# Kernel optimization log

Hardware: AMD Instinct MI355X
Metric: run time of the kernel (lower is better)

The kernel has to match this reference:

```python
import jax, jax.numpy as jnp
import numpy as np

B, S, D, E2 = 64, 512, 1024, 1024  # batch, enc seq len, dec hidden, 2*enc hidden


def setup_inputs() -> dict:
    key = jax.random.key(0)
    ks = jax.random.split(key, 5)
    scale = 1.0 / np.sqrt(D + E2)
    return {
        "dec_state": jax.random.normal(ks[0], (B, D), jnp.float32),
        "enc_states": jax.random.normal(ks[1], (B, S, E2), jnp.float32),
        "att_mask": jnp.ones((B, S), jnp.int32),
        "w_weight": jax.random.normal(ks[2], (D, D + E2), jnp.float32) * scale,
        "w_bias": jax.random.normal(ks[3], (D,), jnp.float32) * scale,
        "v_weight": jax.random.normal(ks[4], (D,), jnp.float32) * (1.0 / np.sqrt(D)),
    }


def reference(dec_state, enc_states, att_mask, w_weight, w_bias, v_weight):
    # Additive (Bahdanau) attention. Split the concat-linear into two GEMMs:
    # tanh(W [dec; enc] + b) == tanh(dec @ Wd^T + enc @ We^T + b) -- same math,
    # avoids materializing the repeated/concatenated [B,S,D+2E] tensor.
    Wd = w_weight[:, :dec_state.shape[-1]]          # [D, D]
    We = w_weight[:, dec_state.shape[-1]:]          # [D, 2E]
    dec_proj = jnp.einsum('bd,kd->bk', dec_state, Wd)        # [B, D]
    enc_proj = jnp.einsum('bse,ke->bsk', enc_states, We)     # [B, S, D]
    energy = jnp.tanh(enc_proj + dec_proj[:, None, :] + w_bias)  # [B, S, D]
    attention = jnp.einsum('bsk,k->bs', energy, v_weight)    # [B, S]
    attention = jnp.where(att_mask == 0, -jnp.inf, attention)
    att_weights = jax.nn.softmax(attention, axis=1)          # [B, S]
    att_out = jnp.einsum('bs,bse->be', att_weights, enc_states)[:, None, :]  # [B,1,2E]
    return att_out
```

## Files before the change

### kernel.cpp

```cpp
#include <hip/hip_runtime.h>
#include <hip/hip_bf16.h>
#include <math.h>

#define B_  64
#define S_  512
#define D_  1024
#define E2_ 1024
#define WROW (D_ + E2_)
#define NTILES 4

typedef __attribute__((ext_vector_type(8))) short bf16x8;
typedef __attribute__((ext_vector_type(4))) float f32x4;
typedef __attribute__((ext_vector_type(8))) unsigned short u16x8;

__device__ __forceinline__ unsigned short f2bf(float f) {
    unsigned u = __float_as_uint(f);
    u = (u + 0x7FFFu + ((u >> 16) & 1u)) >> 16;
    return (unsigned short)u;
}

__device__ __forceinline__ void load_lds16(const void* g, void* l) {
    __builtin_amdgcn_global_load_lds(
        (__attribute__((address_space(1))) void*)(void*)g,
        (__attribute__((address_space(3))) void*)l,
        16, 0, 0);
}

__device__ __forceinline__ float fast_tanh(float x) {
    float ax = fminf(fabsf(x), 16.0f);
    float t  = __builtin_amdgcn_exp2f(ax * 2.8853900817779268f);
    float r  = (t - 1.0f) * __builtin_amdgcn_rcpf(t + 1.0f);
    return copysignf(r, x);
}

__global__ __launch_bounds__(256) void conv_we_kernel(
        const float* __restrict__ w, unsigned short* __restrict__ web)
{
    const int k = blockIdx.x;
    const int j = threadIdx.x * 4;
    float4 a = *reinterpret_cast<const float4*>(w + (size_t)k * WROW + D_ + j);
    ushort4 o;
    o.x = f2bf(a.x); o.y = f2bf(a.y); o.z = f2bf(a.z); o.w = f2bf(a.w);
    *reinterpret_cast<ushort4*>(web + (size_t)k * E2_ + j) = o;
}

__global__ __launch_bounds__(256) void dec_proj_kernel(
        const float* __restrict__ dec,
        const float* __restrict__ w,
        const float* __restrict__ bias,
        float* __restrict__ t)
{
    __shared__ float wrow[D_];
    __shared__ float red[256];
    const int k = blockIdx.x;
    const int tid = threadIdx.x;

    const float* wr = w + (size_t)k * WROW;
    for (int i = tid; i < D_; i += 256) wrow[i] = wr[i];
    __syncthreads();

    const int b = tid >> 2;
    const int q = tid & 3;
    const float* dp = dec + b * D_ + q * 256;
    const float* wp = wrow + q * 256;
    float acc = 0.f;
    #pragma unroll 8
    for (int i = 0; i < 256; ++i) acc = fmaf(dp[i], wp[i], acc);
    red[tid] = acc;
    __syncthreads();
    if (q == 0) {
        float s = red[tid] + red[tid + 1] + red[tid + 2] + red[tid + 3];
        t[b * D_ + k] = s + bias[k];
    }
}

#define BME 256
#define BNE 256
#define BKE 64
#define KT_ (E2_ / BKE)

__global__ __launch_bounds__(512, 2) void energy_mfma_kernel(
        const float* __restrict__ encf,
        const unsigned short* __restrict__ web,
        const float* __restrict__ t,
        const float* __restrict__ v,
        float* __restrict__ att_part)
{
    __shared__ __align__(16) unsigned short As[2][BME * BKE];
    __shared__ __align__(16) unsigned short Bs[2][BNE * BKE];
    __shared__ float tv_s[BNE];
    __shared__ float vv_s[BNE];
    __shared__ float red[4][BME];

    const int g     = blockIdx.x;
    const int mblk  = (g & 7) + 8 * (g >> 5);
    const int ntile = (g >> 3) & 3;

    const int m0 = mblk * BME;
    const int n0 = ntile * BNE;
    const int b  = m0 >> 9;
    const int tid = threadIdx.x;
    const int w   = tid >> 6;
    const int l   = tid & 63;
    const int wm  = w >> 2;
    const int wn  = w & 3;

    if (tid < BNE) {
        tv_s[tid] = t[b * D_ + n0 + tid];
        vv_s[tid] = v[n0 + tid];
    }

    const int arow0 = tid >> 4;
    const int acolb = (tid & 15) * 8;
    const int aswz  = (arow0 & 7) << 4;
    const float* gAf = encf + (size_t)m0 * E2_;

    const int lr8 = l >> 3;
    const int lk  = 8 * ((l & 7) ^ lr8);
    const unsigned short* gB = web + (size_t)n0 * E2_;

    const int rA = wm * 128 + (l & 15);
    const int rB = wn * 64 + (l & 15);
    const int kswz = (l & 7) << 4;
    const int khi  = (l >> 4) << 4;

    f32x4 acc[8][4] = {};
    float4 av[8];

    auto issueA = [&](int kt) {
        const int k0 = kt * BKE;
        #pragma unroll
        for (int i = 0; i < 8; ++i) {
            const int row = i * 32 + arow0;
            av[i] = *reinterpret_cast<const float4*>(
                gAf + (size_t)row * E2_ + k0 + (tid & 15) * 4);
        }
    };
    auto writeA = [&](int bf) {
        #pragma unroll
        for (int i = 0; i < 8; ++i) {
            const int row = i * 32 + arow0;
            unsigned p0, p1;
            asm("v_cvt_pk_bf16_f32 %0, %1, %2"
                : "=v"(p0) : "v"(av[i].x), "v"(av[i].y));
            asm("v_cvt_pk_bf16_f32 %0, %1, %2"
                : "=v"(p1) : "v"(av[i].z), "v"(av[i].w));
            uint2 o; o.x = p0; o.y = p1;
            *reinterpret_cast<uint2*>(
                (char*)As[bf] + row * 128 + (acolb ^ aswz)) = o;
        }
    };
    auto issueB = [&](int bf, int kt) {
        const int k0 = kt * BKE;
        #pragma unroll
        for (int r = 0; r < 4; ++r) {
            const int c = r * 8 + w;
            const int row = c * 8 + lr8;
            load_lds16(gB + (size_t)row * E2_ + k0 + lk,
                       (char*)Bs[bf] + c * 1024);
        }
    };

    issueA(0);
    issueB(0, 0);
    writeA(0);
    issueA(1);
    asm volatile("s_waitcnt vmcnt(8) lgkmcnt(0)" ::: "memory");
    __builtin_amdgcn_s_barrier();
    __builtin_amdgcn_sched_barrier(0);

    for (int kt = 0; kt < KT_; ++kt) {
        const int cur = kt & 1;
        const int nxt = cur ^ 1;

        if (kt + 1 < KT_) issueB(nxt, kt + 1);
        __builtin_amdgcn_sched_barrier(0);

        {
            const int kb = khi ^ kswz;
            bf16x8 a[8], bb[4];
            #pragma unroll
            for (int mi = 0; mi < 8; ++mi)
                a[mi] = *reinterpret_cast<const bf16x8*>(
                    (const char*)As[cur] + (rA + mi * 16) * 128 + kb);
            #pragma unroll
            for (int ni = 0; ni < 4; ++ni)
                bb[ni] = *reinterpret_cast<const bf16x8*>(
                    (const char*)Bs[cur] + (rB + ni * 16) * 128 + kb);
            __builtin_amdgcn_s_setprio(1);
            #pragma unroll
            for (int mi = 0; mi < 8; ++mi)
                #pragma unroll
                for (int ni = 0; ni < 4; ++ni)
                    acc[mi][ni] = __builtin_amdgcn_mfma_f32_16x16x32_bf16(
                        a[mi], bb[ni], acc[mi][ni], 0, 0, 0);
            __builtin_amdgcn_s_setprio(0);
        }
        __builtin_amdgcn_sched_barrier(0);

        if (kt + 1 < KT_) writeA(nxt);
        if (kt + 2 < KT_) issueA(kt + 2);
        __builtin_amdgcn_sched_barrier(0);

        {
            const int kb = (64 + khi) ^ kswz;
            bf16x8 a[8], bb[4];
            #pragma unroll
            for (int mi = 0; mi < 8; ++mi)
                a[mi] = *reinterpret_cast<const bf16x8*>(
                    (const char*)As[cur] + (rA + mi * 16) * 128 + kb);
            #pragma unroll
            for (int ni = 0; ni < 4; ++ni)
                bb[ni] = *reinterpret_cast<const bf16x8*>(
                    (const char*)Bs[cur] + (rB + ni * 16) * 128 + kb);
            __builtin_amdgcn_s_setprio(1);
            #pragma unroll
            for (int mi = 0; mi < 8; ++mi)
                #pragma unroll
                for (int ni = 0; ni < 4; ++ni)
                    acc[mi][ni] = __builtin_amdgcn_mfma_f32_16x16x32_bf16(
                        a[mi], bb[ni], acc[mi][ni], 0, 0, 0);
            __builtin_amdgcn_s_setprio(0);
        }
        __builtin_amdgcn_sched_barrier(0);

        if (kt + 2 < KT_) {
            asm volatile("s_waitcnt vmcnt(8) lgkmcnt(0)" ::: "memory");
        } else if (kt + 1 < KT_) {
            asm volatile("s_waitcnt vmcnt(0) lgkmcnt(0)" ::: "memory");
        }
        __builtin_amdgcn_s_barrier();
        __builtin_amdgcn_sched_barrier(0);
    }

    #pragma unroll
    for (int mi = 0; mi < 8; ++mi) {
        float P[4] = {0.f, 0.f, 0.f, 0.f};
        #pragma unroll
        for (int ni = 0; ni < 4; ++ni) {
            const int nl = wn * 64 + ni * 16 + (l & 15);
            const float tvv = tv_s[nl];
            const float vvv = vv_s[nl];
            #pragma unroll
            for (int j = 0; j < 4; ++j) {
                float e = fast_tanh(acc[mi][ni][j] + tvv);
                P[j] = fmaf(e, vvv, P[j]);
            }
        }
        #pragma unroll
        for (int j = 0; j < 4; ++j) {
            float p = P[j];
            p += __shfl_xor(p, 1);
            p += __shfl_xor(p, 2);
            p += __shfl_xor(p, 4);
            p += __shfl_xor(p, 8);
            if ((l & 15) == 0)
                red[wn][wm * 128 + mi * 16 + (l >> 4) * 4 + j] = p;
        }
    }
    __syncthreads();
    if (tid < BME)
        att_part[(size_t)(m0 + tid) * NTILES + ntile] =
            (red[0][tid] + red[1][tid]) + (red[2][tid] + red[3][tid]);
}

__global__ __launch_bounds__(256) void softmax_kernel(
        const float* __restrict__ att_part,
        const int* __restrict__ mask,
        float* __restrict__ wout)
{
    __shared__ float red[256];
    const int b = blockIdx.x;
    const int tid = threadIdx.x;

    float x0 = 0.f, x1 = 0.f;
    #pragma unroll
    for (int p = 0; p < NTILES; ++p) {
        x0 += att_part[(size_t)(b * S_ + tid) * NTILES + p];
        x1 += att_part[(size_t)(b * S_ + 256 + tid) * NTILES + p];
    }
    bool m0v = (mask[b * S_ + tid] != 0);
    bool m1v = (mask[b * S_ + 256 + tid] != 0);
    if (!m0v) x0 = -INFINITY;
    if (!m1v) x1 = -INFINITY;

    float m = fmaxf(x0, x1);
    red[tid] = m;
    __syncthreads();
    for (int o = 128; o > 0; o >>= 1) {
        if (tid < o) red[tid] = fmaxf(red[tid], red[tid + o]);
        __syncthreads();
    }
    m = red[0];
    __syncthreads();

    float e0 = m0v ? expf(x0 - m) : 0.f;
    float e1 = m1v ? expf(x1 - m) : 0.f;
    red[tid] = e0 + e1;
    __syncthreads();
    for (int o = 128; o > 0; o >>= 1) {
        if (tid < o) red[tid] += red[tid + o];
        __syncthreads();
    }
    const float inv = 1.f / red[0];
    wout[b * S_ + tid] = e0 * inv;
    wout[b * S_ + 256 + tid] = e1 * inv;
}

__global__ __launch_bounds__(256) void attout_part_kernel(
        const float* __restrict__ wgt,
        const float* __restrict__ enc,
        float* __restrict__ out_part)
{
    __shared__ float wsm[64];
    const int b  = blockIdx.y;
    const int sc = blockIdx.x;
    const int tid = threadIdx.x;
    if (tid < 64) wsm[tid] = wgt[b * S_ + sc * 64 + tid];
    __syncthreads();

    const float4* ep = reinterpret_cast<const float4*>(
        enc + ((size_t)b * S_ + sc * 64) * E2_) + tid;
    float4 acc = {0.f, 0.f, 0.f, 0.f};
    #pragma unroll 8
    for (int s = 0; s < 64; ++s) {
        float4 e4 = ep[(size_t)s * (E2_ / 4)];
        const float ws = wsm[s];
        acc.x = fmaf(ws, e4.x, acc.x);
        acc.y = fmaf(ws, e4.y, acc.y);
        acc.z = fmaf(ws, e4.z, acc.z);
        acc.w = fmaf(ws, e4.w, acc.w);
    }
    reinterpret_cast<float4*>(out_part + ((size_t)sc * B_ + b) * E2_)[tid] = acc;
}

__global__ __launch_bounds__(256) void attout_reduce_kernel(
        const float* __restrict__ out_part,
        float* __restrict__ out)
{
    const int idx = blockIdx.x * 256 + threadIdx.x;
    const int n4 = (B_ * E2_) / 4;
    const float4* p = reinterpret_cast<const float4*>(out_part);
    float4 r = p[idx];
    #pragma unroll
    for (int c = 1; c < 8; ++c) {
        float4 q = p[idx + c * n4];
        r.x += q.x; r.y += q.y; r.z += q.z; r.w += q.w;
    }
    reinterpret_cast<float4*>(out)[idx] = r;
}

extern "C" void kernel_launch(void* const* d_in, const int* in_sizes, int n_in,
                              void* d_out, int out_size, void* d_ws, size_t ws_size,
                              hipStream_t stream) {
    const float* dec  = (const float*)d_in[0];
    const float* enc  = (const float*)d_in[1];
    const int*   mask = (const int*)d_in[2];
    const float* w    = (const float*)d_in[3];
    const float* bias = (const float*)d_in[4];
    const float* v    = (const float*)d_in[5];
    float* out = (float*)d_out;

    float* t_buf    = (float*)d_ws;
    float* att_part = t_buf + B_ * D_;
    float* wgt_buf  = att_part + B_ * S_ * NTILES;
    float* out_part = wgt_buf + B_ * S_;
    unsigned short* web = (unsigned short*)(out_part + 8 * B_ * E2_);

    conv_we_kernel<<<D_, 256, 0, stream>>>(w, web);
    dec_proj_kernel<<<D_, 256, 0, stream>>>(dec, w, bias, t_buf);
    energy_mfma_kernel<<<512, 512, 0, stream>>>(enc, web, t_buf, v, att_part);
    softmax_kernel<<<B_, 256, 0, stream>>>(att_part, mask, wgt_buf);
    attout_part_kernel<<<dim3(8, B_), 256, 0, stream>>>(wgt_buf, enc, out_part);
    attout_reduce_kernel<<<(B_ * E2_ / 4) / 256, 256, 0, stream>>>(out_part, out);
}
```

Before: 143.1 us.

## Fuse prep kernels, write bf16 enc copy in energy GEMM, fuse softmax into attout

Merges the weight conversion and dec projection into one launch and folds the softmax into the attention-output kernel, which recomputes it per block. The energy GEMM now writes a bf16 copy of enc_states from its ntile==0 blocks, so the weighted sum reads half the bytes. It also drops the min-blocks hint from the GEMM launch bounds. This removes two launches and cuts the second full read of enc, at the cost of extra global stores inside the GEMM, a possible register or occupancy change, and bf16 rounding in the output sum.

```diff
diff --git a/kernel.cpp b/kernel.cpp
--- a/kernel.cpp
+++ b/kernel.cpp
@@ -19,6 +19,10 @@
     return (unsigned short)u;
 }
 
+__device__ __forceinline__ float bf2f(unsigned short u) {
+    return __uint_as_float((unsigned)u << 16);
+}
+
 __device__ __forceinline__ void load_lds16(const void* g, void* l) {
     __builtin_amdgcn_global_load_lds(
         (__attribute__((address_space(1))) void*)(void*)g,
@@ -33,44 +37,44 @@
     return copysignf(r, x);
 }
 
-__global__ __launch_bounds__(256) void conv_we_kernel(
-        const float* __restrict__ w, unsigned short* __restrict__ web)
-{
-    const int k = blockIdx.x;
-    const int j = threadIdx.x * 4;
-    float4 a = *reinterpret_cast<const float4*>(w + (size_t)k * WROW + D_ + j);
-    ushort4 o;
-    o.x = f2bf(a.x); o.y = f2bf(a.y); o.z = f2bf(a.z); o.w = f2bf(a.w);
-    *reinterpret_cast<ushort4*>(web + (size_t)k * E2_ + j) = o;
-}
-
-__global__ __launch_bounds__(256) void dec_proj_kernel(
+__global__ __launch_bounds__(256) void prep_kernel(
+        const float* __restrict__ w,
         const float* __restrict__ dec,
-        const float* __restrict__ w,
         const float* __restrict__ bias,
+        unsigned short* __restrict__ web,
         float* __restrict__ t)
 {
-    __shared__ float wrow[D_];
-    __shared__ float red[256];
-    const int k = blockIdx.x;
+    const int blk = blockIdx.x;
     const int tid = threadIdx.x;
 
-    const float* wr = w + (size_t)k * WROW;
-    for (int i = tid; i < D_; i += 256) wrow[i] = wr[i];
-    __syncthreads();
-
-    const int b = tid >> 2;
-    const int q = tid & 3;
-    const float* dp = dec + b * D_ + q * 256;
-    const float* wp = wrow + q * 256;
-    float acc = 0.f;
-    #pragma unroll 8
-    for (int i = 0; i < 256; ++i) acc = fmaf(dp[i], wp[i], acc);
-    red[tid] = acc;
-    __syncthreads();
-    if (q == 0) {
-        float s = red[tid] + red[tid + 1] + red[tid + 2] + red[tid + 3];
-        t[b * D_ + k] = s + bias[k];
+    if (blk < D_) {
+        const int k = blk;
+        const int j = tid * 4;
+        float4 a = *reinterpret_cast<const float4*>(w + (size_t)k * WROW + D_ + j);
+        ushort4 o;
+        o.x = f2bf(a.x); o.y = f2bf(a.y); o.z = f2bf(a.z); o.w = f2bf(a.w);
+        *reinterpret_cast<ushort4*>(web + (size_t)k * E2_ + j) = o;
+    } else {
+        __shared__ float wrow[D_];
+        __shared__ float red[256];
+        const int k = blk - D_;
+        const float* wr = w + (size_t)k * WROW;
+        for (int i = tid; i < D_; i += 256) wrow[i] = wr[i];
+        __syncthreads();
+
+        const int b = tid >> 2;
+        const int q = tid & 3;
+        const float* dp = dec + b * D_ + q * 256;
+        const float* wp = wrow + q * 256;
+        float acc = 0.f;
+        #pragma unroll 8
+        for (int i = 0; i < 256; ++i) acc = fmaf(dp[i], wp[i], acc);
+        red[tid] = acc;
+        __syncthreads();
+        if (q == 0) {
+            float s = red[tid] + red[tid + 1] + red[tid + 2] + red[tid + 3];
+            t[b * D_ + k] = s + bias[k];
+        }
     }
 }
 
@@ -79,12 +83,13 @@
 #define BKE 64
 #define KT_ (E2_ / BKE)
 
-__global__ __launch_bounds__(512, 2) void energy_mfma_kernel(
+__global__ __launch_bounds__(512) void energy_mfma_kernel(
         const float* __restrict__ encf,
         const unsigned short* __restrict__ web,
         const float* __restrict__ t,
         const float* __restrict__ v,
-        float* __restrict__ att_part)
+        float* __restrict__ att_part,
+        unsigned short* __restrict__ encb)
 {
     __shared__ __align__(16) unsigned short As[2][BME * BKE];
     __shared__ __align__(16) unsigned short Bs[2][BNE * BKE];
@@ -104,6 +109,7 @@
     const int l   = tid & 63;
     const int wm  = w >> 2;
     const int wn  = w & 3;
+    const bool do_store = (ntile == 0);
 
     if (tid < BNE) {
         tv_s[tid] = t[b * D_ + n0 + tid];
@@ -114,6 +120,7 @@
     const int acolb = (tid & 15) * 8;
     const int aswz  = (arow0 & 7) << 4;
     const float* gAf = encf + (size_t)m0 * E2_;
+    unsigned short* gOut = encb + (size_t)m0 * E2_;
 
     const int lr8 = l >> 3;
     const int lk  = 8 * ((l & 7) ^ lr8);
@@ -136,7 +143,8 @@
                 gAf + (size_t)row * E2_ + k0 + (tid & 15) * 4);
         }
     };
-    auto writeA = [&](int bf) {
+    auto writeA = [&](int bf, int kt) {
+        const int k0 = kt * BKE;
         #pragma unroll
         for (int i = 0; i < 8; ++i) {
             const int row = i * 32 + arow0;
@@ -148,6 +156,9 @@
             uint2 o; o.x = p0; o.y = p1;
             *reinterpret_cast<uint2*>(
                 (char*)As[bf] + row * 128 + (acolb ^ aswz)) = o;
+            if (do_store)
+                *reinterpret_cast<uint2*>(
+                    gOut + (size_t)row * E2_ + k0 + (tid & 15) * 4) = o;
         }
     };
     auto issueB = [&](int bf, int kt) {
@@ -163,7 +174,7 @@
 
     issueA(0);
     issueB(0, 0);
-    writeA(0);
+    writeA(0, 0);
     issueA(1);
     asm volatile("s_waitcnt vmcnt(8) lgkmcnt(0)" ::: "memory");
     __builtin_amdgcn_s_barrier();
@@ -198,7 +209,7 @@
         }
         __builtin_amdgcn_sched_barrier(0);
 
-        if (kt + 1 < KT_) writeA(nxt);
+        if (kt + 1 < KT_) writeA(nxt, kt + 1);
         if (kt + 2 < KT_) issueA(kt + 2);
         __builtin_amdgcn_sched_barrier(0);
 
@@ -264,74 +275,70 @@
             (red[0][tid] + red[1][tid]) + (red[2][tid] + red[3][tid]);
 }
 
-__global__ __launch_bounds__(256) void softmax_kernel(
+__global__ __launch_bounds__(128) void attout_sm_kernel(
         const float* __restrict__ att_part,
         const int* __restrict__ mask,
-        float* __restrict__ wout)
-{
-    __shared__ float red[256];
-    const int b = blockIdx.x;
-    const int tid = threadIdx.x;
-
-    float x0 = 0.f, x1 = 0.f;
-    #pragma unroll
-    for (int p = 0; p < NTILES; ++p) {
-        x0 += att_part[(size_t)(b * S_ + tid) * NTILES + p];
-        x1 += att_part[(size_t)(b * S_ + 256 + tid) * NTILES + p];
-    }
-    bool m0v = (mask[b * S_ + tid] != 0);
-    bool m1v = (mask[b * S_ + 256 + tid] != 0);
-    if (!m0v) x0 = -INFINITY;
-    if (!m1v) x1 = -INFINITY;
-
-    float m = fmaxf(x0, x1);
-    red[tid] = m;
-    __syncthreads();
-    for (int o = 128; o > 0; o >>= 1) {
-        if (tid < o) red[tid] = fmaxf(red[tid], red[tid + o]);
-        __syncthreads();
-    }
-    m = red[0];
-    __syncthreads();
-
-    float e0 = m0v ? expf(x0 - m) : 0.f;
-    float e1 = m1v ? expf(x1 - m) : 0.f;
-    red[tid] = e0 + e1;
-    __syncthreads();
-    for (int o = 128; o > 0; o >>= 1) {
-        if (tid < o) red[tid] += red[tid + o];
-        __syncthreads();
-    }
-    const float inv = 1.f / red[0];
-    wout[b * S_ + tid] = e0 * inv;
-    wout[b * S_ + 256 + tid] = e1 * inv;
-}
-
-__global__ __launch_bounds__(256) void attout_part_kernel(
-        const float* __restrict__ wgt,
-        const float* __restrict__ enc,
+        const unsigned short* __restrict__ encb,
         float* __restrict__ out_part)
 {
-    __shared__ float wsm[64];
+    __shared__ float wall[S_];
+    __shared__ float red[128];
     const int b  = blockIdx.y;
     const int sc = blockIdx.x;
     const int tid = threadIdx.x;
-    if (tid < 64) wsm[tid] = wgt[b * S_ + sc * 64 + tid];
-    __syncthreads();
-
-    const float4* ep = reinterpret_cast<const float4*>(
-        enc + ((size_t)b * S_ + sc * 64) * E2_) + tid;
-    float4 acc = {0.f, 0.f, 0.f, 0.f};
-    #pragma unroll 8
+
+    float x[4];
+    bool mv[4];
+    #pragma unroll
+    for (int j = 0; j < 4; ++j) {
+        const int s = tid + j * 128;
+        float4 p = *reinterpret_cast<const float4*>(
+            att_part + (size_t)(b * S_ + s) * NTILES);
+        x[j] = (p.x + p.y) + (p.z + p.w);
+        mv[j] = (mask[b * S_ + s] != 0);
+        if (!mv[j]) x[j] = -INFINITY;
+    }
+    float m = fmaxf(fmaxf(x[0], x[1]), fmaxf(x[2], x[3]));
+    red[tid] = m;
+    __syncthreads();
+    for (int o = 64; o > 0; o >>= 1) {
+        if (tid < o) red[tid] = fmaxf(red[tid], red[tid + o]);
+        __syncthreads();
+    }
+    m = red[0];
+    __syncthreads();
+    float e[4], esum = 0.f;
+    #pragma unroll
+    for (int j = 0; j < 4; ++j) {
+        e[j] = mv[j] ? expf(x[j] - m) : 0.f;
+        esum += e[j];
+    }
+    red[tid] = esum;
+    __syncthreads();
+    for (int o = 64; o > 0; o >>= 1) {
+        if (tid < o) red[tid] += red[tid + o];
+        __syncthreads();
+    }
+    const float inv = 1.f / red[0];
+    #pragma unroll
+    for (int j = 0; j < 4; ++j) wall[tid + j * 128] = e[j] * inv;
+    __syncthreads();
+
+    const float* wsm = wall + sc * 64;
+    const unsigned short* ep =
+        encb + ((size_t)b * S_ + sc * 64) * E2_ + tid * 8;
+    float acc[8] = {};
+    #pragma unroll 4
     for (int s = 0; s < 64; ++s) {
-        float4 e4 = ep[(size_t)s * (E2_ / 4)];
+        u16x8 e8 = *reinterpret_cast<const u16x8*>(ep + (size_t)s * E2_);
         const float ws = wsm[s];
-        acc.x = fmaf(ws, e4.x, acc.x);
-        acc.y = fmaf(ws, e4.y, acc.y);
-        acc.z = fmaf(ws, e4.z, acc.z);
-        acc.w = fmaf(ws, e4.w, acc.w);
-    }
-    reinterpret_cast<float4*>(out_part + ((size_t)sc * B_ + b) * E2_)[tid] = acc;
+        #pragma unroll
+        for (int j = 0; j < 8; ++j)
+            acc[j] = fmaf(ws, bf2f((unsigned short)e8[j]), acc[j]);
+    }
+    float* op = out_part + ((size_t)sc * B_ + b) * E2_ + tid * 8;
+    #pragma unroll
+    for (int j = 0; j < 8; ++j) op[j] = acc[j];
 }
 
 __global__ __launch_bounds__(256) void attout_reduce_kernel(
@@ -363,14 +370,14 @@
 
     float* t_buf    = (float*)d_ws;
     float* att_part = t_buf + B_ * D_;
-    float* wgt_buf  = att_part + B_ * S_ * NTILES;
-    float* out_part = wgt_buf + B_ * S_;
-    unsigned short* web = (unsigned short*)(out_part + 8 * B_ * E2_);
-
-    conv_we_kernel<<<D_, 256, 0, stream>>>(w, web);
-    dec_proj_kernel<<<D_, 256, 0, stream>>>(dec, w, bias, t_buf);
-    energy_mfma_kernel<<<512, 512, 0, stream>>>(enc, web, t_buf, v, att_part);
-    softmax_kernel<<<B_, 256, 0, stream>>>(att_part, mask, wgt_buf);
-    attout_part_kernel<<<dim3(8, B_), 256, 0, stream>>>(wgt_buf, enc, out_part);
+    float* out_part = att_part + B_ * S_ * NTILES;
+    unsigned short* web  = (unsigned short*)(out_part + 8 * B_ * E2_);
+    unsigned short* encb = web + (size_t)D_ * E2_;
+
+    prep_kernel<<<2 * D_, 256, 0, stream>>>(w, dec, bias, web, t_buf);
+    energy_mfma_kernel<<<512, 512, 0, stream>>>(enc, web, t_buf, v,
+                                                att_part, encb);
+    attout_sm_kernel<<<dim3(8, B_), 128, 0, stream>>>(att_part, mask,
+                                                      encb, out_part);
     attout_reduce_kernel<<<(B_ * E2_ / 4) / 256, 256, 0, stream>>>(out_part, out);
 }
```

Result: no change. 141.5 us (-1.1%).

## Merge prep kernels and fuse softmax into attention-output partial kernel

Applied to the files above, without the earlier changes.

Combines the weight bf16 conversion and the decoder projection into one launch, with each block choosing its role from its index. Folds the softmax into the attention-output partial kernel: every (chunk, batch) block recomputes the full-row softmax in shared memory, which removes the separate softmax launch and the weight buffer round trip. It also vectorises the partial-score loads and drops the min-blocks-per-CU hint on the energy GEMM. The cost is that the softmax is computed redundantly eight times per batch row, and the GEMM may end up with different register allocation and occupancy.

```diff
diff --git a/kernel.cpp b/kernel.cpp
--- a/kernel.cpp
+++ b/kernel.cpp
@@ -33,44 +33,44 @@
     return copysignf(r, x);
 }
 
-__global__ __launch_bounds__(256) void conv_we_kernel(
-        const float* __restrict__ w, unsigned short* __restrict__ web)
-{
-    const int k = blockIdx.x;
-    const int j = threadIdx.x * 4;
-    float4 a = *reinterpret_cast<const float4*>(w + (size_t)k * WROW + D_ + j);
-    ushort4 o;
-    o.x = f2bf(a.x); o.y = f2bf(a.y); o.z = f2bf(a.z); o.w = f2bf(a.w);
-    *reinterpret_cast<ushort4*>(web + (size_t)k * E2_ + j) = o;
-}
-
-__global__ __launch_bounds__(256) void dec_proj_kernel(
+__global__ __launch_bounds__(256) void prep_kernel(
+        const float* __restrict__ w,
         const float* __restrict__ dec,
-        const float* __restrict__ w,
         const float* __restrict__ bias,
+        unsigned short* __restrict__ web,
         float* __restrict__ t)
 {
-    __shared__ float wrow[D_];
-    __shared__ float red[256];
-    const int k = blockIdx.x;
+    const int blk = blockIdx.x;
     const int tid = threadIdx.x;
 
-    const float* wr = w + (size_t)k * WROW;
-    for (int i = tid; i < D_; i += 256) wrow[i] = wr[i];
-    __syncthreads();
-
-    const int b = tid >> 2;
-    const int q = tid & 3;
-    const float* dp = dec + b * D_ + q * 256;
-    const float* wp = wrow + q * 256;
-    float acc = 0.f;
-    #pragma unroll 8
-    for (int i = 0; i < 256; ++i) acc = fmaf(dp[i], wp[i], acc);
-    red[tid] = acc;
-    __syncthreads();
-    if (q == 0) {
-        float s = red[tid] + red[tid + 1] + red[tid + 2] + red[tid + 3];
-        t[b * D_ + k] = s + bias[k];
+    if (blk < D_) {
+        const int k = blk;
+        const int j = tid * 4;
+        float4 a = *reinterpret_cast<const float4*>(w + (size_t)k * WROW + D_ + j);
+        ushort4 o;
+        o.x = f2bf(a.x); o.y = f2bf(a.y); o.z = f2bf(a.z); o.w = f2bf(a.w);
+        *reinterpret_cast<ushort4*>(web + (size_t)k * E2_ + j) = o;
+    } else {
+        __shared__ float wrow[D_];
+        __shared__ float red[256];
+        const int k = blk - D_;
+        const float* wr = w + (size_t)k * WROW;
+        for (int i = tid; i < D_; i += 256) wrow[i] = wr[i];
+        __syncthreads();
+
+        const int b = tid >> 2;
+        const int q = tid & 3;
+        const float* dp = dec + b * D_ + q * 256;
+        const float* wp = wrow + q * 256;
+        float acc = 0.f;
+        #pragma unroll 8
+        for (int i = 0; i < 256; ++i) acc = fmaf(dp[i], wp[i], acc);
+        red[tid] = acc;
+        __syncthreads();
+        if (q == 0) {
+            float s = red[tid] + red[tid + 1] + red[tid + 2] + red[tid + 3];
+            t[b * D_ + k] = s + bias[k];
+        }
     }
 }
 
@@ -79,7 +79,7 @@
 #define BKE 64
 #define KT_ (E2_ / BKE)
 
-__global__ __launch_bounds__(512, 2) void energy_mfma_kernel(
+__global__ __launch_bounds__(512) void energy_mfma_kernel(
         const float* __restrict__ encf,
         const unsigned short* __restrict__ web,
         const float* __restrict__ t,
@@ -264,27 +264,30 @@
             (red[0][tid] + red[1][tid]) + (red[2][tid] + red[3][tid]);
 }
 
-__global__ __launch_bounds__(256) void softmax_kernel(
+__global__ __launch_bounds__(256) void attout_sm_kernel(
         const float* __restrict__ att_part,
         const int* __restrict__ mask,
-        float* __restrict__ wout)
+        const float* __restrict__ enc,
+        float* __restrict__ out_part)
 {
+    __shared__ float wall[S_];
     __shared__ float red[256];
-    const int b = blockIdx.x;
+    const int b  = blockIdx.y;
+    const int sc = blockIdx.x;
     const int tid = threadIdx.x;
 
-    float x0 = 0.f, x1 = 0.f;
+    float x[2];
+    bool mv[2];
     #pragma unroll
-    for (int p = 0; p < NTILES; ++p) {
-        x0 += att_part[(size_t)(b * S_ + tid) * NTILES + p];
-        x1 += att_part[(size_t)(b * S_ + 256 + tid) * NTILES + p];
-    }
-    bool m0v = (mask[b * S_ + tid] != 0);
-    bool m1v = (mask[b * S_ + 256 + tid] != 0);
-    if (!m0v) x0 = -INFINITY;
-    if (!m1v) x1 = -INFINITY;
-
-    float m = fmaxf(x0, x1);
+    for (int j = 0; j < 2; ++j) {
+        const int s = tid + j * 256;
+        float4 p = *reinterpret_cast<const float4*>(
+            att_part + (size_t)(b * S_ + s) * NTILES);
+        x[j] = (p.x + p.y) + (p.z + p.w);
+        mv[j] = (mask[b * S_ + s] != 0);
+        if (!mv[j]) x[j] = -INFINITY;
+    }
+    float m = fmaxf(x[0], x[1]);
     red[tid] = m;
     __syncthreads();
     for (int o = 128; o > 0; o >>= 1) {
@@ -293,9 +296,8 @@
     }
     m = red[0];
     __syncthreads();
-
-    float e0 = m0v ? expf(x0 - m) : 0.f;
-    float e1 = m1v ? expf(x1 - m) : 0.f;
+    float e0 = mv[0] ? expf(x[0] - m) : 0.f;
+    float e1 = mv[1] ? expf(x[1] - m) : 0.f;
     red[tid] = e0 + e1;
     __syncthreads();
     for (int o = 128; o > 0; o >>= 1) {
@@ -303,22 +305,11 @@
         __syncthreads();
     }
     const float inv = 1.f / red[0];
-    wout[b * S_ + tid] = e0 * inv;
-    wout[b * S_ + 256 + tid] = e1 * inv;
-}
-
-__global__ __launch_bounds__(256) void attout_part_kernel(
-        const float* __restrict__ wgt,
-        const float* __restrict__ enc,
-        float* __restrict__ out_part)
-{
-    __shared__ float wsm[64];
-    const int b  = blockIdx.y;
-    const int sc = blockIdx.x;
-    const int tid = threadIdx.x;
-    if (tid < 64) wsm[tid] = wgt[b * S_ + sc * 64 + tid];
-    __syncthreads();
-
+    wall[tid] = e0 * inv;
+    wall[tid + 256] = e1 * inv;
+    __syncthreads();
+
+    const float* wsm = wall + sc * 64;
     const float4* ep = reinterpret_cast<const float4*>(
         enc + ((size_t)b * S_ + sc * 64) * E2_) + tid;
     float4 acc = {0.f, 0.f, 0.f, 0.f};
@@ -363,14 +354,12 @@
 
     float* t_buf    = (float*)d_ws;
     float* att_part = t_buf + B_ * D_;
-    float* wgt_buf  = att_part + B_ * S_ * NTILES;
-    float* out_part = wgt_buf + B_ * S_;
+    float* out_part = att_part + B_ * S_ * NTILES;
     unsigned short* web = (unsigned short*)(out_part + 8 * B_ * E2_);
 
-    conv_we_kernel<<<D_, 256, 0, stream>>>(w, web);
-    dec_proj_kernel<<<D_, 256, 0, stream>>>(dec, w, bias, t_buf);
+    prep_kernel<<<2 * D_, 256, 0, stream>>>(w, dec, bias, web, t_buf);
     energy_mfma_kernel<<<512, 512, 0, stream>>>(enc, web, t_buf, v, att_part);
-    softmax_kernel<<<B_, 256, 0, stream>>>(att_part, mask, wgt_buf);
-    attout_part_kernel<<<dim3(8, B_), 256, 0, stream>>>(wgt_buf, enc, out_part);
+    attout_sm_kernel<<<dim3(8, B_), 256, 0, stream>>>(att_part, mask,
+                                                      enc, out_part);
     attout_reduce_kernel<<<(B_ * E2_ / 4) / 256, 256, 0, stream>>>(out_part, out);
 }
```

Measured after the change: 137.3 us. -4.1%, faster.
